# Kernel tuning notes

Measured on AMD Instinct MI355X. Metric: run time of the kernel, lower is better.

The kernel has to match this reference:

```python
import jax, jax.numpy as jnp
import numpy as np


def setup_inputs() -> dict:
    key = jax.random.key(0)
    k1, k2 = jax.random.split(key)
    x = jax.random.normal(k1, (8, 256, 64, 64), dtype=jnp.float32)
    # 1x1 conv weight, no bias: [out_c, in_c]
    W = jax.random.normal(k2, (256, 256), dtype=jnp.float32) * (1.0 / np.sqrt(256.0))
    return {"x": x, "W": W}


def reference(x, W):
    b, c, h, w = x.shape
    n = h * w
    xf = x.reshape(b, c, n)  # [b, c, N]
    scale = jnp.asarray(c, x.dtype) ** -0.5
    # sim_map[b, i, j] = sum_c q[b,i,c] * k[b,c,j], q = k = x tokens
    sim = jnp.einsum('bci,bcj->bij', xf, xf) * scale  # [b, N, N]
    attn = jax.nn.softmax(sim, axis=-1)
    # context = attn @ value, then back to [b, c, N]
    ctx = jnp.einsum('bij,bcj->bci', attn, xf)  # [b, c, N]
    ctx = ctx.reshape(b, c, h, w)
    # 1x1 conv, bias-free == channel matmul
    out = jnp.einsum('oc,bchw->bohw', W, ctx)
    return out
```

## Files before the change

kernel.cpp:

```cpp
#include <hip/hip_runtime.h>


typedef __attribute__((ext_vector_type(8))) short short8;
typedef __attribute__((ext_vector_type(4))) float floatx4;
typedef __attribute__((ext_vector_type(16))) float floatx16;
typedef __attribute__((ext_vector_type(4))) int intx4;
typedef __attribute__((ext_vector_type(8))) int intx8;

#define N_TOK 4096
#define C_DIM 256
#define JT 64
#define NT 32
#define SC 0.09016844005556021f

typedef const __attribute__((address_space(1))) unsigned int g_uint;
typedef __attribute__((address_space(3))) unsigned int lds_uint;

__device__ __forceinline__ void gll16(const void* g, void* l) {
  __builtin_amdgcn_global_load_lds((g_uint*)g, (lds_uint*)l, 16, 0, 0);
}

__device__ __forceinline__ unsigned short f2bf(float f) {
  unsigned int u = __builtin_bit_cast(unsigned int, f);
  u += 0x7fffu + ((u >> 16) & 1u);
  return (unsigned short)(u >> 16);
}
__device__ __forceinline__ float bf2f(unsigned short v) {
  return __builtin_bit_cast(float, (unsigned int)v << 16);
}
__device__ __forceinline__ unsigned char f2f8(float f) {
  unsigned u = __builtin_bit_cast(unsigned, f);
  unsigned sgn = (u >> 24) & 0x80u;
  unsigned a = u & 0x7fffffffu;
  if (a > 0x43e40000u) return (unsigned char)(sgn | 0x7e);
  unsigned lsb = (a >> 20) & 1u;
  a += 0x0007ffffu + lsb;
  int e = (int)(a >> 23) - 127;
  if (e < -6) return (unsigned char)sgn;
  if (e > 8) return (unsigned char)(sgn | 0x7e);
  unsigned m = (a >> 20) & 7u;
  return (unsigned char)(sgn | ((unsigned)(e + 7) << 3) | m);
}
__device__ __forceinline__ float f8dec(unsigned b) {
  unsigned s = (b & 0x80u) << 24;
  unsigned e = (b >> 3) & 15u;
  unsigned m = b & 7u;
  if (e)
    return __builtin_bit_cast(float, s | ((e + 120u) << 23) | (m << 20));
  float sub = (float)m * 0.001953125f;
  return (b & 0x80u) ? -sub : sub;
}

__device__ __forceinline__ floatx4 mfma16(short8 a, short8 b, floatx4 c) {
  return __builtin_amdgcn_mfma_f32_16x16x32_bf16(a, b, c, 0, 0, 0);
}
__device__ __forceinline__ floatx16 mfma8(intx8 a, intx8 b, floatx16 c) {
  return __builtin_amdgcn_mfma_scale_f32_32x32x64_f8f6f4(
      a, b, c, 0, 0, 0, 0x7f7f7f7f, 0, 0x7f7f7f7f);
}
template <bool HI>
__device__ __forceinline__ int pk_fp8(float a, float b, int old) {
#if __has_builtin(__builtin_amdgcn_cvt_pk_fp8_f32)
  return __builtin_amdgcn_cvt_pk_fp8_f32(a, b, old, HI);
#else
  unsigned w = (unsigned)f2f8(a) | ((unsigned)f2f8(b) << 8);
  return HI ? (int)(((unsigned)old & 0x0000ffffu) | (w << 16))
            : (int)(((unsigned)old & 0xffff0000u) | w);
#endif
}


__global__ __launch_bounds__(256) void transpose_conv(
    const float* __restrict__ x, unsigned char* __restrict__ xT8,
    unsigned char* __restrict__ xC8p, unsigned short* __restrict__ resid) {
  __shared__ float tile[32][33];
  const int b = blockIdx.z;
  const int i0 = blockIdx.x * 32, c0 = blockIdx.y * 32;
  const int tx = threadIdx.x & 31, ty = threadIdx.x >> 5;
  const float* xb = x + (size_t)b * C_DIM * N_TOK;
#pragma unroll
  for (int p = 0; p < 4; ++p) {
    int c = c0 + ty + p * 8;
    float v = xb[(size_t)c * N_TOK + i0 + tx];
    tile[ty + p * 8][tx] = v;
    int j = i0 + tx, jg = j & 63;
    int kp = ((jg >> 2) & 1) * 32 + ((jg >> 5) & 1) * 16 + ((jg >> 3) & 3) * 4 + (jg & 3);
    xC8p[((size_t)b * C_DIM + c) * N_TOK + (j & ~63) + kp] = f2f8(v);
  }
  __syncthreads();
#pragma unroll
  for (int p = 0; p < 4; ++p) {
    int i = i0 + ty + p * 8;
    float v = tile[tx][ty + p * 8];
    unsigned char q8 = f2f8(v);
    size_t idx = ((size_t)b * N_TOK + i) * C_DIM + c0 + tx;
    xT8[idx] = q8;
    resid[idx] = f2bf(v - f8dec(q8));
  }
}

__global__ __launch_bounds__(256) void wconv(const float* __restrict__ W,
                                             unsigned short* __restrict__ Wb) {
  int idx = blockIdx.x * 256 + threadIdx.x;
  Wb[idx] = f2bf(W[idx]);
}

__global__ __launch_bounds__(256) void mrow_kernel(
    const unsigned char* __restrict__ xT8, float* __restrict__ Mrow) {
  const int row = blockIdx.x * 4 + (threadIdx.x >> 6);
  const int lane = threadIdx.x & 63;
  const unsigned char* rp = xT8 + (size_t)row * C_DIM + lane * 4;
  float s = 0.f;
#pragma unroll
  for (int e = 0; e < 4; ++e) {
    float v = f8dec(rp[e]);
    s += v * v;
  }
  s += __shfl_xor(s, 1);
  s += __shfl_xor(s, 2);
  s += __shfl_xor(s, 4);
  s += __shfl_xor(s, 8);
  s += __shfl_xor(s, 16);
  s += __shfl_xor(s, 32);
  if (lane == 0) Mrow[row] = s * SC;
}

__global__ __launch_bounds__(256, 2) void attn_kernel(
    const unsigned char* __restrict__ xT8, const unsigned char* __restrict__ xC8p,
    const float* __restrict__ Mrow, unsigned short* __restrict__ ctxP,
    float* __restrict__ Ld) {
  const int bid = blockIdx.x;
  const int b = bid & 7;
  const int qt = (bid >> 3) & 31;
  const int g = bid >> 8;
  const int tid = threadIdx.x;
  const int lane = tid & 63;
  const int wv = tid >> 6;
  const int l31 = lane & 31;
  const int h = lane >> 5;
  const unsigned char* xT8b = xT8 + (size_t)b * N_TOK * C_DIM;
  const unsigned char* xCb = xC8p + (size_t)b * C_DIM * N_TOK;
  const int qb = qt * 128 + wv * 32;

  __shared__ char lds[2][32768];

  const char* kBase;
  {
    int j0 = wv * 4 + (lane >> 4);
    int c16 = (lane & 15) ^ (j0 & 15);
    kBase = (const char*)xT8b + (size_t)g * 2048 * 256 + j0 * 256 + c16 * 16;
  }
  const char* vBase;
  {
    int c0 = wv * 16 + (lane >> 2);
    int kv = (lane & 3) ^ ((lane >> 3) & 3);
    vBase = (const char*)xCb + (size_t)c0 * N_TOK + g * 2048 + kv * 16;
  }
  auto STAGE_K = [&](int t, int sel) {
    char* Kd = lds[sel] + wv * 1024;
    const char* src = kBase + (size_t)t * 16384;
#pragma unroll
    for (int i = 0; i < 4; ++i) gll16(src + i * 4096, Kd + i * 4096);
  };
  auto STAGE_V = [&](int t, int sel) {
    char* Vd = lds[sel] + 16384 + wv * 1024;
    const char* src = vBase + (size_t)t * 64;
#pragma unroll
    for (int i = 0; i < 4; ++i) gll16(src + (size_t)i * 64 * N_TOK, Vd + i * 4096);
  };

  intx8 q[4];
  {
    const unsigned char* qp = xT8b + (size_t)(qb + l31) * C_DIM + h * 32;
#pragma unroll
    for (int ks = 0; ks < 4; ++ks) {
      intx4 lo = *(const intx4*)(qp + ks * 64);
      intx4 hi = *(const intx4*)(qp + ks * 64 + 16);
      q[ks] = (intx8){lo.x, lo.y, lo.z, lo.w, hi.x, hi.y, hi.z, hi.w};
    }
  }
  const float mi = Mrow[(size_t)b * N_TOK + qb + l31];

  const int a0 = l31 * 64 + (((2 * h) ^ ((l31 >> 1) & 3)) << 4);

  floatx16 acc[8];
#pragma unroll
  for (int ct = 0; ct < 8; ++ct)
#pragma unroll
    for (int r = 0; r < 16; ++r) acc[ct][r] = 0.f;
  float lsum = 0.f;

  STAGE_K(0, 0);
  STAGE_V(0, 0);

  for (int t = 0; t < NT; ++t) {
    __syncthreads();
    if (t + 1 < NT) {
      STAGE_K(t + 1, (t + 1) & 1);
      STAGE_V(t + 1, (t + 1) & 1);
    }
    const char* Kb = lds[t & 1];
    const char* Vb = lds[t & 1] + 16384;

    floatx16 s0, s1;
#pragma unroll
    for (int r = 0; r < 16; ++r) { s0[r] = 0.f; s1[r] = 0.f; }
    __builtin_amdgcn_s_setprio(1);
#pragma unroll
    for (int ks = 0; ks < 4; ++ks) {
      int ch = ((ks * 4 + h * 2) ^ (l31 & 15)) << 4;
      intx4 ka = *(const intx4*)(Kb + l31 * 256 + ch);
      intx4 kb2 = *(const intx4*)(Kb + l31 * 256 + (ch ^ 16));
      intx8 kf = (intx8){ka.x, ka.y, ka.z, ka.w, kb2.x, kb2.y, kb2.z, kb2.w};
      s0 = mfma8(kf, q[ks], s0);
      ka = *(const intx4*)(Kb + (32 + l31) * 256 + ch);
      kb2 = *(const intx4*)(Kb + (32 + l31) * 256 + (ch ^ 16));
      kf = (intx8){ka.x, ka.y, ka.z, ka.w, kb2.x, kb2.y, kb2.z, kb2.w};
      s1 = mfma8(kf, q[ks], s1);
    }
    __builtin_amdgcn_s_setprio(0);

#pragma unroll
    for (int r = 0; r < 16; ++r) {
      s0[r] = exp2f(s0[r] * SC - mi);
      s1[r] = exp2f(s1[r] * SC - mi);
      lsum += s0[r] + s1[r];
    }

    int pk[8];
#pragma unroll
    for (int i = 0; i < 4; ++i) {
      int v = pk_fp8<false>(s0[4 * i], s0[4 * i + 1], 0);
      pk[i] = pk_fp8<true>(s0[4 * i + 2], s0[4 * i + 3], v);
      v = pk_fp8<false>(s1[4 * i], s1[4 * i + 1], 0);
      pk[4 + i] = pk_fp8<true>(s1[4 * i + 2], s1[4 * i + 3], v);
    }

    intx8 pa = (intx8){pk[0], pk[1], pk[2], pk[3], pk[4], pk[5], pk[6], pk[7]};
    __builtin_amdgcn_s_setprio(1);
#pragma unroll
    for (int ct = 0; ct < 8; ++ct) {
      const char* vp = Vb + ct * 2048;
      intx4 lo = *(const intx4*)(vp + a0);
      intx4 hi = *(const intx4*)(vp + (a0 ^ 16));
      intx8 vf = (intx8){lo.x, lo.y, lo.z, lo.w, hi.x, hi.y, hi.z, hi.w};
      acc[ct] = mfma8(pa, vf, acc[ct]);
    }
    __builtin_amdgcn_s_setprio(0);
  }

  lsum += __shfl_xor(lsum, 32);
  if (h == 0) Ld[((size_t)g * 8 + b) * N_TOK + qb + l31] = lsum;
  unsigned short* cb = ctxP + (((size_t)g * 8 + b) * N_TOK + qb) * C_DIM;
#pragma unroll
  for (int r = 0; r < 16; ++r) {
    int ri = (r & 3) + 8 * (r >> 2) + 4 * h;
#pragma unroll
    for (int ct = 0; ct < 8; ++ct)
      cb[(size_t)ri * C_DIM + ct * 32 + l31] = f2bf(acc[ct][r]);
  }
}

__global__ __launch_bounds__(256) void outgemm(
    const unsigned short* __restrict__ ctxP, const unsigned short* __restrict__ Wb,
    const float* __restrict__ Ld, const unsigned short* __restrict__ resid,
    float* __restrict__ out) {
  const int bid = blockIdx.x;
  const int b = bid & 7;
  const int it = bid >> 3;
  const int lane = threadIdx.x & 63;
  const int w = threadIdx.x >> 6;
  const int ibase = it * 64 + w * 16;
  const int l15 = lane & 15, lhi = lane >> 4;
  const unsigned short* c0base = ctxP + (size_t)b * N_TOK * C_DIM;
  const unsigned short* c1base = ctxP + (size_t)(8 + b) * N_TOK * C_DIM;
  const float* l0b = Ld + (size_t)b * N_TOK;
  const float* l1b = Ld + (size_t)(8 + b) * N_TOK;

  const int ia = ibase + l15;
  const unsigned short* rrow = resid + (((size_t)b * N_TOK + ia) * C_DIM);

  float rden[4];
#pragma unroll
  for (int r = 0; r < 4; ++r) {
    int is = ibase + lhi * 4 + r;
    rden[r] = 1.0f / (l0b[is] + l1b[is]);
  }

  floatx4 acc[16];
#pragma unroll
  for (int i = 0; i < 16; ++i) acc[i] = (floatx4){0.f, 0.f, 0.f, 0.f};

#pragma unroll
  for (int ks = 0; ks < 8; ++ks) {
    short8 o0 = *(const short8*)(c0base + (size_t)ia * C_DIM + ks * 32 + lhi * 8);
    short8 o1 = *(const short8*)(c1base + (size_t)ia * C_DIM + ks * 32 + lhi * 8);
    short8 rs = *(const short8*)(rrow + ks * 32 + lhi * 8);
    short8 am;
#pragma unroll
    for (int e = 0; e < 8; ++e)
      am[e] = (short)f2bf(bf2f((unsigned short)o0[e]) +
                          bf2f((unsigned short)o1[e]) +
                          bf2f((unsigned short)rs[e]));
#pragma unroll
    for (int ob = 0; ob < 16; ++ob) {
      short8 bw = *(const short8*)(Wb + (size_t)(ob * 16 + l15) * C_DIM + ks * 32 + lhi * 8);
      acc[ob] = mfma16(am, bw, acc[ob]);
    }
  }
  float* outb = out + (size_t)b * C_DIM * N_TOK;
#pragma unroll
  for (int ob = 0; ob < 16; ++ob) {
#pragma unroll
    for (int r = 0; r < 4; ++r) {
      int o = ob * 16 + l15;
      int i = ibase + lhi * 4 + r;
      outb[(size_t)o * N_TOK + i] = acc[ob][r] * rden[r];
    }
  }
}

extern "C" void kernel_launch(void* const* d_in, const int* in_sizes, int n_in,
                              void* d_out, int out_size, void* d_ws, size_t ws_size,
                              hipStream_t stream) {
  const float* x = (const float*)d_in[0];
  const float* W = (const float*)d_in[1];
  float* out = (float*)d_out;
  char* ws = (char*)d_ws;
  const size_t SZ8 = (size_t)8 * N_TOK * C_DIM;
  const size_t SZ = SZ8 * 2;
  unsigned char* xT8 = (unsigned char*)(ws);
  unsigned char* xC8p = (unsigned char*)(ws + SZ8);
  unsigned short* resid = (unsigned short*)(ws + 2 * SZ8);
  unsigned short* ctxP = (unsigned short*)(ws + 2 * SZ8 + SZ);
  unsigned short* Wb = (unsigned short*)(ws + 2 * SZ8 + 3 * SZ);
  float* Ld = (float*)(ws + 2 * SZ8 + 3 * SZ + C_DIM * C_DIM * 2);
  float* Mrow = (float*)(ws + 2 * SZ8 + 3 * SZ + C_DIM * C_DIM * 2 + 262144);

  hipLaunchKernelGGL(transpose_conv, dim3(N_TOK / 32, C_DIM / 32, 8), dim3(256), 0,
                     stream, x, xT8, xC8p, resid);
  hipLaunchKernelGGL(wconv, dim3((C_DIM * C_DIM) / 256), dim3(256), 0, stream, W, Wb);
  hipLaunchKernelGGL(mrow_kernel, dim3(8 * N_TOK / 4), dim3(256), 0, stream, xT8, Mrow);
  hipLaunchKernelGGL(attn_kernel, dim3(512), dim3(256), 0, stream, xT8, xC8p, Mrow,
                     ctxP, Ld);
  hipLaunchKernelGGL(outgemm, dim3(512), dim3(256), 0, stream, ctxP, Wb, Ld, resid, out);
}
```

Before: 144.9 us.

## Fuse split-KV reduction and output 1x1 conv GEMM into attention kernel

The two key-split halves of attention are now computed by two wave groups inside one 512-thread block. Their partial context and row sums are combined through LDS, normalized with the residual added, and then multiplied by the conv weight with 32x32 bf16 MFMAs in the same kernel. This removes the bf16 ctxP/Ld round trip through global memory and one kernel launch. In exchange, the grid halves to 256 blocks at one block per CU using 128KB of LDS, which lowers occupancy and latency hiding in the main attention loop.

```diff
diff --git a/kernel.cpp b/kernel.cpp
--- a/kernel.cpp
+++ b/kernel.cpp
@@ -51,8 +51,8 @@
   return (b & 0x80u) ? -sub : sub;
 }
 
-__device__ __forceinline__ floatx4 mfma16(short8 a, short8 b, floatx4 c) {
-  return __builtin_amdgcn_mfma_f32_16x16x32_bf16(a, b, c, 0, 0, 0);
+__device__ __forceinline__ floatx16 mfma32(short8 a, short8 b, floatx16 c) {
+  return __builtin_amdgcn_mfma_f32_32x32x16_bf16(a, b, c, 0, 0, 0);
 }
 __device__ __forceinline__ floatx16 mfma8(intx8 a, intx8 b, floatx16 c) {
   return __builtin_amdgcn_mfma_scale_f32_32x32x64_f8f6f4(
@@ -69,6 +69,10 @@
 #endif
 }
 
+__device__ __forceinline__ int ctx_byte(int I, int c) {
+  return I * 512 + ((((c >> 3) ^ (I & 31))) << 4) + (c & 7) * 2;
+}
+
 
 __global__ __launch_bounds__(256) void transpose_conv(
     const float* __restrict__ x, unsigned char* __restrict__ xT8,
@@ -125,45 +129,48 @@
   if (lane == 0) Mrow[row] = s * SC;
 }
 
-__global__ __launch_bounds__(256, 2) void attn_kernel(
+__global__ __launch_bounds__(512, 1) void attn_kernel(
     const unsigned char* __restrict__ xT8, const unsigned char* __restrict__ xC8p,
-    const float* __restrict__ Mrow, unsigned short* __restrict__ ctxP,
-    float* __restrict__ Ld) {
+    const float* __restrict__ Mrow, const unsigned short* __restrict__ resid,
+    const unsigned short* __restrict__ Wb, float* __restrict__ out) {
   const int bid = blockIdx.x;
   const int b = bid & 7;
-  const int qt = (bid >> 3) & 31;
-  const int g = bid >> 8;
+  const int qt = bid >> 3;
   const int tid = threadIdx.x;
   const int lane = tid & 63;
   const int wv = tid >> 6;
+  const int wg = wv & 3;
+  const int grp = wv >> 2;
   const int l31 = lane & 31;
   const int h = lane >> 5;
   const unsigned char* xT8b = xT8 + (size_t)b * N_TOK * C_DIM;
   const unsigned char* xCb = xC8p + (size_t)b * C_DIM * N_TOK;
-  const int qb = qt * 128 + wv * 32;
-
-  __shared__ char lds[2][32768];
+  const int qb = qt * 128 + wg * 32;
+
+  __shared__ char lds[131072];
+  __shared__ float lbuf[2][128];
+  char* gbase = lds + grp * 65536;
 
   const char* kBase;
   {
-    int j0 = wv * 4 + (lane >> 4);
+    int j0 = wg * 4 + (lane >> 4);
     int c16 = (lane & 15) ^ (j0 & 15);
-    kBase = (const char*)xT8b + (size_t)g * 2048 * 256 + j0 * 256 + c16 * 16;
+    kBase = (const char*)xT8b + (size_t)grp * 2048 * 256 + j0 * 256 + c16 * 16;
   }
   const char* vBase;
   {
-    int c0 = wv * 16 + (lane >> 2);
+    int c0 = wg * 16 + (lane >> 2);
     int kv = (lane & 3) ^ ((lane >> 3) & 3);
-    vBase = (const char*)xCb + (size_t)c0 * N_TOK + g * 2048 + kv * 16;
+    vBase = (const char*)xCb + (size_t)c0 * N_TOK + grp * 2048 + kv * 16;
   }
   auto STAGE_K = [&](int t, int sel) {
-    char* Kd = lds[sel] + wv * 1024;
+    char* Kd = gbase + sel * 32768 + wg * 1024;
     const char* src = kBase + (size_t)t * 16384;
 #pragma unroll
     for (int i = 0; i < 4; ++i) gll16(src + i * 4096, Kd + i * 4096);
   };
   auto STAGE_V = [&](int t, int sel) {
-    char* Vd = lds[sel] + 16384 + wv * 1024;
+    char* Vd = gbase + sel * 32768 + 16384 + wg * 1024;
     const char* src = vBase + (size_t)t * 64;
 #pragma unroll
     for (int i = 0; i < 4; ++i) gll16(src + (size_t)i * 64 * N_TOK, Vd + i * 4096);
@@ -180,7 +187,6 @@
     }
   }
   const float mi = Mrow[(size_t)b * N_TOK + qb + l31];
-
   const int a0 = l31 * 64 + (((2 * h) ^ ((l31 >> 1) & 3)) << 4);
 
   floatx16 acc[8];
@@ -199,8 +205,8 @@
       STAGE_K(t + 1, (t + 1) & 1);
       STAGE_V(t + 1, (t + 1) & 1);
     }
-    const char* Kb = lds[t & 1];
-    const char* Vb = lds[t & 1] + 16384;
+    const char* Kb = gbase + (t & 1) * 32768;
+    const char* Vb = Kb + 16384;
 
     floatx16 s0, s1;
 #pragma unroll
@@ -250,72 +256,67 @@
   }
 
   lsum += __shfl_xor(lsum, 32);
-  if (h == 0) Ld[((size_t)g * 8 + b) * N_TOK + qb + l31] = lsum;
-  unsigned short* cb = ctxP + (((size_t)g * 8 + b) * N_TOK + qb) * C_DIM;
-#pragma unroll
-  for (int r = 0; r < 16; ++r) {
-    int ri = (r & 3) + 8 * (r >> 2) + 4 * h;
-#pragma unroll
-    for (int ct = 0; ct < 8; ++ct)
-      cb[(size_t)ri * C_DIM + ct * 32 + l31] = f2bf(acc[ct][r]);
-  }
-}
-
-__global__ __launch_bounds__(256) void outgemm(
-    const unsigned short* __restrict__ ctxP, const unsigned short* __restrict__ Wb,
-    const float* __restrict__ Ld, const unsigned short* __restrict__ resid,
-    float* __restrict__ out) {
-  const int bid = blockIdx.x;
-  const int b = bid & 7;
-  const int it = bid >> 3;
-  const int lane = threadIdx.x & 63;
-  const int w = threadIdx.x >> 6;
-  const int ibase = it * 64 + w * 16;
-  const int l15 = lane & 15, lhi = lane >> 4;
-  const unsigned short* c0base = ctxP + (size_t)b * N_TOK * C_DIM;
-  const unsigned short* c1base = ctxP + (size_t)(8 + b) * N_TOK * C_DIM;
-  const float* l0b = Ld + (size_t)b * N_TOK;
-  const float* l1b = Ld + (size_t)(8 + b) * N_TOK;
-
-  const int ia = ibase + l15;
-  const unsigned short* rrow = resid + (((size_t)b * N_TOK + ia) * C_DIM);
-
-  float rden[4];
-#pragma unroll
-  for (int r = 0; r < 4; ++r) {
-    int is = ibase + lhi * 4 + r;
-    rden[r] = 1.0f / (l0b[is] + l1b[is]);
-  }
-
-  floatx4 acc[16];
-#pragma unroll
-  for (int i = 0; i < 16; ++i) acc[i] = (floatx4){0.f, 0.f, 0.f, 0.f};
-
-#pragma unroll
-  for (int ks = 0; ks < 8; ++ks) {
-    short8 o0 = *(const short8*)(c0base + (size_t)ia * C_DIM + ks * 32 + lhi * 8);
-    short8 o1 = *(const short8*)(c1base + (size_t)ia * C_DIM + ks * 32 + lhi * 8);
-    short8 rs = *(const short8*)(rrow + ks * 32 + lhi * 8);
-    short8 am;
-#pragma unroll
-    for (int e = 0; e < 8; ++e)
-      am[e] = (short)f2bf(bf2f((unsigned short)o0[e]) +
-                          bf2f((unsigned short)o1[e]) +
-                          bf2f((unsigned short)rs[e]));
-#pragma unroll
-    for (int ob = 0; ob < 16; ++ob) {
-      short8 bw = *(const short8*)(Wb + (size_t)(ob * 16 + l15) * C_DIM + ks * 32 + lhi * 8);
-      acc[ob] = mfma16(am, bw, acc[ob]);
-    }
-  }
+  __syncthreads();
+  if (h == 0) lbuf[grp][wg * 32 + l31] = lsum;
+  if (grp == 1) {
+#pragma unroll
+    for (int r = 0; r < 16; ++r) {
+      int I = wg * 32 + (r & 3) + 8 * (r >> 2) + 4 * h;
+#pragma unroll
+      for (int ct = 0; ct < 8; ++ct) {
+        int c = ct * 32 + l31;
+        *(unsigned short*)(lds + 65536 + ctx_byte(I, c)) = f2bf(acc[ct][r]);
+      }
+    }
+  }
+  __syncthreads();
+  if (grp == 0) {
+    const unsigned short* rbase = resid + ((size_t)b * N_TOK + qt * 128) * C_DIM;
+#pragma unroll
+    for (int r = 0; r < 16; ++r) {
+      int I = wg * 32 + (r & 3) + 8 * (r >> 2) + 4 * h;
+      float linv = 1.0f / (lbuf[0][I] + lbuf[1][I]);
+#pragma unroll
+      for (int ct = 0; ct < 8; ++ct) {
+        int c = ct * 32 + l31;
+        float pv = bf2f(*(const unsigned short*)(lds + 65536 + ctx_byte(I, c)));
+        float rv = bf2f(rbase[(size_t)I * C_DIM + c]);
+        *(unsigned short*)(lds + ctx_byte(I, c)) =
+            f2bf((acc[ct][r] + pv + rv) * linv);
+      }
+    }
+  }
+  __syncthreads();
+
+  floatx16 oacc[4];
+#pragma unroll
+  for (int og = 0; og < 4; ++og)
+#pragma unroll
+    for (int r = 0; r < 16; ++r) oacc[og][r] = 0.f;
+  const int Irow = wg * 32 + l31;
+  __builtin_amdgcn_s_setprio(1);
+#pragma unroll
+  for (int ks = 0; ks < 16; ++ks) {
+    short8 cfrag = *(const short8*)(lds + Irow * 512 +
+                                    (((ks * 2 + h) ^ (Irow & 31)) << 4));
+#pragma unroll
+    for (int og = 0; og < 4; ++og) {
+      const unsigned short* wp =
+          Wb + (size_t)(grp * 128 + og * 32 + l31) * C_DIM + ks * 16 + h * 8;
+      short8 wfrag = *(const short8*)wp;
+      oacc[og] = mfma32(wfrag, cfrag, oacc[og]);
+    }
+  }
+  __builtin_amdgcn_s_setprio(0);
   float* outb = out + (size_t)b * C_DIM * N_TOK;
-#pragma unroll
-  for (int ob = 0; ob < 16; ++ob) {
-#pragma unroll
-    for (int r = 0; r < 4; ++r) {
-      int o = ob * 16 + l15;
-      int i = ibase + lhi * 4 + r;
-      outb[(size_t)o * N_TOK + i] = acc[ob][r] * rden[r];
+  const int iglob = qt * 128 + wg * 32 + l31;
+#pragma unroll
+  for (int og = 0; og < 4; ++og) {
+    int o0 = grp * 128 + og * 32;
+#pragma unroll
+    for (int r = 0; r < 16; ++r) {
+      int o = o0 + (r & 3) + 8 * (r >> 2) + 4 * h;
+      outb[(size_t)o * N_TOK + iglob] = oacc[og][r];
     }
   }
 }
@@ -328,20 +329,16 @@
   float* out = (float*)d_out;
   char* ws = (char*)d_ws;
   const size_t SZ8 = (size_t)8 * N_TOK * C_DIM;
-  const size_t SZ = SZ8 * 2;
   unsigned char* xT8 = (unsigned char*)(ws);
   unsigned char* xC8p = (unsigned char*)(ws + SZ8);
   unsigned short* resid = (unsigned short*)(ws + 2 * SZ8);
-  unsigned short* ctxP = (unsigned short*)(ws + 2 * SZ8 + SZ);
-  unsigned short* Wb = (unsigned short*)(ws + 2 * SZ8 + 3 * SZ);
-  float* Ld = (float*)(ws + 2 * SZ8 + 3 * SZ + C_DIM * C_DIM * 2);
-  float* Mrow = (float*)(ws + 2 * SZ8 + 3 * SZ + C_DIM * C_DIM * 2 + 262144);
+  unsigned short* Wb = (unsigned short*)(ws + 4 * SZ8);
+  float* Mrow = (float*)(ws + 4 * SZ8 + C_DIM * C_DIM * 2);
 
   hipLaunchKernelGGL(transpose_conv, dim3(N_TOK / 32, C_DIM / 32, 8), dim3(256), 0,
                      stream, x, xT8, xC8p, resid);
   hipLaunchKernelGGL(wconv, dim3((C_DIM * C_DIM) / 256), dim3(256), 0, stream, W, Wb);
   hipLaunchKernelGGL(mrow_kernel, dim3(8 * N_TOK / 4), dim3(256), 0, stream, xT8, Mrow);
-  hipLaunchKernelGGL(attn_kernel, dim3(512), dim3(256), 0, stream, xT8, xC8p, Mrow,
-                     ctxP, Ld);
-  hipLaunchKernelGGL(outgemm, dim3(512), dim3(256), 0, stream, ctxP, Wb, Ld, resid, out);
-}
+  hipLaunchKernelGGL(attn_kernel, dim3(256), dim3(512), 0, stream, xT8, xC8p, Mrow,
+                     resid, Wb, out);
+}
```

New measurement: 150.7 us. 1.04x slower.
